# Optimization experiments

Measured on AMD Instinct MI355X. Metric: run time of the kernel, lower is better.

## Reference

```python
import jax, jax.numpy as jnp
import numpy as np
from jax import lax

SCALE = 1.0 / np.sqrt(1500.0)  # self.dim = sqrt(1500)


def conv1d(x, w, b, stride, padding):
    # x: [B, Cin, L], w: [Cout, Cin, K] (torch layout)
    y = lax.conv_general_dilated(x, w, (stride,), padding,
                                 dimension_numbers=('NCH', 'OIH', 'NCH'))
    return y + b[None, :, None]


def setup_inputs() -> dict:
    key = jax.random.key(0)
    ks = jax.random.split(key, 16)
    B, L, F = 32, 1500, 8  # feature_len = 8, seq len pinned by sqrt(1500) and logit=Linear(176,3)

    def n(k, shape, s=0.1):
        return jax.random.normal(k, shape, jnp.float32) * s

    return {
        'signal': jax.random.normal(ks[0], (B, 1, L), jnp.float32),
        # first (and only executed) head: kernel_size = 3, padding 'same'
        'wq': n(ks[1], (F, 1, 3)), 'bq': n(ks[2], (F,)),
        'wk': n(ks[3], (F, 1, 3)), 'bk': n(ks[4], (F,)),
        'wv': n(ks[5], (F, 1, 3)), 'bv': n(ks[6], (F,)),
        # final conv stack (finetune path): 1500 -> 374 -> 92 -> 22
        'w1': n(ks[7], (32, F, 8)),  'b1': n(ks[8], (32,)),
        'w2': n(ks[9], (64, 32, 8)), 'b2': n(ks[10], (64,)),
        'w3': n(ks[11], (F, 64, 8)), 'b3': n(ks[12], (F,)),
        # logit: Linear(176, 3); 176 = 8 * 22
        'wl': n(ks[13], (3, 176)), 'bl': n(ks[14], (3,)),
    }


def reference(signal, wq, bq, wk, bk, wv, bv, w1, b1, w2, b2, w3, b3, wl, bl):
    # conv QKV projections (kernel 3, 'same' padding), each [B, 8, L]
    Q = conv1d(signal, wq, bq, 1, 'SAME')
    K = conv1d(signal, wk, bk, 1, 'SAME')
    V = conv1d(signal, wv, bv, 1, 'SAME')
    # score = bmm(Q^T, K) / sqrt(1500)  -> [B, L, L]
    score = jnp.einsum('bcl,bcm->blm', Q, K) * SCALE
    attn = jax.nn.softmax(score, axis=-1)
    # context = bmm(attn, V^T)^T -> [B, 8, L]
    context = jnp.einsum('blm,bcm->bcl', attn, V)
    # finetune head: three strided convs (no activations in the original)
    h = conv1d(context, w1, b1, 4, 'VALID')  # [B, 32, 374]
    h = conv1d(h, w2, b2, 4, 'VALID')        # [B, 64, 92]
    h = conv1d(h, w3, b3, 4, 'VALID')        # [B, 8, 22]
    flat = h.reshape(h.shape[0], -1)          # [B, 176]
    return flat @ wl.T + bl                   # [B, 3]
```

## Files before the change

### kernel.cpp

```cpp
#include <hip/hip_runtime.h>

#define F_SCALE 0.02581988897471611f
#define F_LOG2E 1.4426950408889634f

constexpr int B_ = 32;
constexpr int L_ = 1500;
constexpr int LP_ = 1504;
constexpr int MSPLIT = 16;
constexpr int MCHUNK = 94;

constexpr size_t OFF_PS   = 0;
constexpr size_t SZ_PS    = (size_t)B_ * MSPLIT * 4 * LP_;
constexpr size_t OFF_CTX  = OFF_PS + SZ_PS;
constexpr size_t SZ_CTX   = (size_t)B_ * 8 * LP_;
constexpr size_t OFF_H1   = OFF_CTX + SZ_CTX;
constexpr size_t SZ_H1    = (size_t)B_ * 32 * 376;
constexpr size_t OFF_H2   = OFF_H1 + SZ_H1;
constexpr size_t SZ_H2    = (size_t)B_ * 64 * 96;

__global__ __launch_bounds__(256, 6) void attn_partial(
    const float* __restrict__ signal,
    const float* __restrict__ wq, const float* __restrict__ bq,
    const float* __restrict__ wk,
    float* __restrict__ ps)
{
    __shared__ float  sigp[LP_];
    __shared__ float4 gArr[MCHUNK];

    const int tid = threadIdx.x;
    const int lt  = blockIdx.x;
    const int ms  = blockIdx.y;
    const int b   = blockIdx.z;
    const int m0  = ms * MCHUNK;
    const int mcount = min(MCHUNK, L_ - m0);

    const float* sgb = signal + (size_t)b * L_;
    for (int i = tid; i < LP_; i += 256)
        sigp[i] = (i >= 1 && i <= L_) ? sgb[i - 1] : 0.0f;

    float Mm[9], uu[3];
    #pragma unroll
    for (int a = 0; a < 3; a++) {
        #pragma unroll
        for (int d = 0; d < 3; d++) {
            float acc = 0.0f;
            #pragma unroll
            for (int c = 0; c < 8; c++) acc += wq[c*3+a] * wk[c*3+d];
            Mm[a*3+d] = acc * (F_SCALE * F_LOG2E);
        }
    }
    #pragma unroll
    for (int d = 0; d < 3; d++) {
        float acc = 0.0f;
        #pragma unroll
        for (int c = 0; c < 8; c++) acc += bq[c] * wk[c*3+d];
        uu[d] = acc * (F_SCALE * F_LOG2E);
    }
    __syncthreads();

    for (int j = tid; j < mcount; j += 256) {
        const int m = m0 + j;
        const float x0 = sigp[m], x1 = sigp[m+1], x2 = sigp[m+2];
        float4 g;
        g.x = Mm[0]*x0 + Mm[1]*x1 + Mm[2]*x2;
        g.y = Mm[3]*x0 + Mm[4]*x1 + Mm[5]*x2;
        g.z = Mm[6]*x0 + Mm[7]*x1 + Mm[8]*x2;
        g.w = uu[0]*x0 + uu[1]*x1 + uu[2]*x2;
        gArr[j] = g;
    }
    __syncthreads();

    const int l0 = lt * 512 + tid;
    const int l1 = l0 + 256;
    const bool has1 = (l1 < L_);
    const int l1c = has1 ? l1 : (L_ - 1);

    const float xa0 = sigp[l0],  xa1 = sigp[l0+1],  xa2 = sigp[l0+2];
    const float xb0 = sigp[l1c], xb1 = sigp[l1c+1], xb2 = sigp[l1c+2];

    float S0a=0,S1a=0,S2a=0,Da=0, S0b=0,S1b=0,S2b=0,Db=0;
    float sa = sigp[m0], sb = sigp[m0+1];

    #pragma unroll 4
    for (int j = 0; j < mcount; j++) {
        const float4 g = gArr[j];
        const float sc = sigp[m0 + j + 2];
        const float s_a = fmaf(xa0, g.x, fmaf(xa1, g.y, fmaf(xa2, g.z, g.w)));
        const float s_b = fmaf(xb0, g.x, fmaf(xb1, g.y, fmaf(xb2, g.z, g.w)));
        const float pa = __builtin_amdgcn_exp2f(s_a);
        const float pb = __builtin_amdgcn_exp2f(s_b);
        Da += pa; Db += pb;
        S0a = fmaf(pa, sa, S0a); S1a = fmaf(pa, sb, S1a); S2a = fmaf(pa, sc, S2a);
        S0b = fmaf(pb, sa, S0b); S1b = fmaf(pb, sb, S1b); S2b = fmaf(pb, sc, S2b);
        sa = sb; sb = sc;
    }

    float* pc = ps + ((size_t)(b * MSPLIT + ms) * 4) * LP_;
    pc[0*LP_+l0]=S0a; pc[1*LP_+l0]=S1a; pc[2*LP_+l0]=S2a; pc[3*LP_+l0]=Da;
    if (has1) {
        pc[0*LP_+l1]=S0b; pc[1*LP_+l1]=S1b; pc[2*LP_+l1]=S2b; pc[3*LP_+l1]=Db;
    }
}

__global__ __launch_bounds__(256) void attn_combine(
    const float* __restrict__ ps,
    const float* __restrict__ wv, const float* __restrict__ bv,
    float* __restrict__ ctx)
{
    const int l = blockIdx.x * 256 + threadIdx.x;
    const int b = blockIdx.y;
    if (l >= L_) return;
    float S0=0, S1=0, S2=0, D=0;
    #pragma unroll
    for (int s = 0; s < MSPLIT; s++) {
        const float* base = ps + ((size_t)(b*MSPLIT + s) * 4) * LP_ + l;
        S0 += base[0*LP_]; S1 += base[1*LP_]; S2 += base[2*LP_]; D += base[3*LP_];
    }
    const float rd = 1.0f / D;
    #pragma unroll
    for (int c = 0; c < 8; c++) {
        ctx[((size_t)b * 8 + c) * LP_ + l] =
            (wv[c*3+0]*S0 + wv[c*3+1]*S1 + wv[c*3+2]*S2) * rd + bv[c];
    }
}

__global__ __launch_bounds__(192) void conv1k(
    const float* __restrict__ ctx, const float* __restrict__ w1,
    const float* __restrict__ b1, float* __restrict__ h1)
{
    const int t = blockIdx.x * 192 + threadIdx.x;
    const int o = blockIdx.y, b = blockIdx.z;
    if (t >= 374) return;
    float acc = b1[o];
    const float4* cb = reinterpret_cast<const float4*>(ctx + (size_t)b * 8 * LP_);
    const float* w = w1 + o * 64;
    #pragma unroll
    for (int i = 0; i < 8; i++) {
        const float4 a0 = cb[i * 376 + t];
        const float4 a1 = cb[i * 376 + t + 1];
        acc += a0.x*w[i*8+0] + a0.y*w[i*8+1] + a0.z*w[i*8+2] + a0.w*w[i*8+3]
             + a1.x*w[i*8+4] + a1.y*w[i*8+5] + a1.z*w[i*8+6] + a1.w*w[i*8+7];
    }
    h1[((size_t)b * 32 + o) * 376 + t] = acc;
}

__global__ __launch_bounds__(128) void conv2k(
    const float* __restrict__ h1, const float* __restrict__ w2,
    const float* __restrict__ b2, float* __restrict__ h2)
{
    const int t = threadIdx.x;
    const int o = blockIdx.x, b = blockIdx.y;
    if (t >= 92) return;
    float acc = b2[o];
    const float4* hb = reinterpret_cast<const float4*>(h1 + (size_t)b * 32 * 376);
    const float* w = w2 + o * 256;
    #pragma unroll 8
    for (int i = 0; i < 32; i++) {
        const float4 a0 = hb[i * 94 + t];
        const float4 a1 = hb[i * 94 + t + 1];
        acc += a0.x*w[i*8+0] + a0.y*w[i*8+1] + a0.z*w[i*8+2] + a0.w*w[i*8+3]
             + a1.x*w[i*8+4] + a1.y*w[i*8+5] + a1.z*w[i*8+6] + a1.w*w[i*8+7];
    }
    h2[((size_t)b * 64 + o) * 96 + t] = acc;
}

__global__ __launch_bounds__(192) void conv3_logit(
    const float* __restrict__ h2, const float* __restrict__ w3,
    const float* __restrict__ b3, const float* __restrict__ wl,
    const float* __restrict__ bl, float* __restrict__ out)
{
    __shared__ float flat[176];
    const int tid = threadIdx.x, b = blockIdx.x;
    if (tid < 176) {
        const int c = tid / 22, t = tid % 22;
        float acc = b3[c];
        const float4* hb = reinterpret_cast<const float4*>(h2 + (size_t)b * 64 * 96);
        #pragma unroll 8
        for (int i = 0; i < 64; i++) {
            const float4 a0 = hb[i * 24 + t];
            const float4 a1 = hb[i * 24 + t + 1];
            const float* w = w3 + (c * 64 + i) * 8;
            acc += a0.x*w[0] + a0.y*w[1] + a0.z*w[2] + a0.w*w[3]
                 + a1.x*w[4] + a1.y*w[5] + a1.z*w[6] + a1.w*w[7];
        }
        flat[tid] = acc;
    }
    __syncthreads();
    if (tid < 3) {
        float acc = bl[tid];
        for (int n = 0; n < 176; n++) acc += flat[n] * wl[tid * 176 + n];
        out[b * 3 + tid] = acc;
    }
}

extern "C" void kernel_launch(void* const* d_in, const int* in_sizes, int n_in,
                              void* d_out, int out_size, void* d_ws, size_t ws_size,
                              hipStream_t stream) {
    const float* signal = (const float*)d_in[0];
    const float* wq = (const float*)d_in[1];  const float* bq = (const float*)d_in[2];
    const float* wk = (const float*)d_in[3];
    const float* wv = (const float*)d_in[5];  const float* bv = (const float*)d_in[6];
    const float* w1 = (const float*)d_in[7];  const float* b1 = (const float*)d_in[8];
    const float* w2 = (const float*)d_in[9];  const float* b2 = (const float*)d_in[10];
    const float* w3 = (const float*)d_in[11]; const float* b3 = (const float*)d_in[12];
    const float* wl = (const float*)d_in[13]; const float* bl = (const float*)d_in[14];
    float* out = (float*)d_out;

    float* ws  = (float*)d_ws;
    float* ps  = ws + OFF_PS;
    float* ctx = ws + OFF_CTX;
    float* h1  = ws + OFF_H1;
    float* h2  = ws + OFF_H2;

    hipLaunchKernelGGL(attn_partial, dim3(3, MSPLIT, 32), dim3(256), 0, stream,
                       signal, wq, bq, wk, ps);
    hipLaunchKernelGGL(attn_combine, dim3(6, 32), dim3(256), 0, stream, ps, wv, bv, ctx);
    hipLaunchKernelGGL(conv1k, dim3(2, 32, 32), dim3(192), 0, stream, ctx, w1, b1, h1);
    hipLaunchKernelGGL(conv2k, dim3(64, 32), dim3(128), 0, stream, h1, w2, b2, h2);
    hipLaunchKernelGGL(conv3_logit, dim3(32), dim3(192), 0, stream, h2, w3, b3, wl, bl, out);
}
```

Baseline: 145.2 us.

## Fuse attention combine with first conv and fold V projection into conv weights

```diff
diff --git a/kernel.cpp b/kernel.cpp
--- a/kernel.cpp
+++ b/kernel.cpp
@@ -11,9 +11,7 @@
 
 constexpr size_t OFF_PS   = 0;
 constexpr size_t SZ_PS    = (size_t)B_ * MSPLIT * 4 * LP_;
-constexpr size_t OFF_CTX  = OFF_PS + SZ_PS;
-constexpr size_t SZ_CTX   = (size_t)B_ * 8 * LP_;
-constexpr size_t OFF_H1   = OFF_CTX + SZ_CTX;
+constexpr size_t OFF_H1   = OFF_PS + SZ_PS;
 constexpr size_t SZ_H1    = (size_t)B_ * 32 * 376;
 constexpr size_t OFF_H2   = OFF_H1 + SZ_H1;
 constexpr size_t SZ_H2    = (size_t)B_ * 64 * 96;
@@ -102,46 +100,68 @@
     }
 }
 
-__global__ __launch_bounds__(256) void attn_combine(
+__global__ __launch_bounds__(256) void fused_ctx_conv1(
     const float* __restrict__ ps,
     const float* __restrict__ wv, const float* __restrict__ bv,
-    float* __restrict__ ctx)
-{
-    const int l = blockIdx.x * 256 + threadIdx.x;
-    const int b = blockIdx.y;
-    if (l >= L_) return;
-    float S0=0, S1=0, S2=0, D=0;
-    #pragma unroll
-    for (int s = 0; s < MSPLIT; s++) {
-        const float* base = ps + ((size_t)(b*MSPLIT + s) * 4) * LP_ + l;
-        S0 += base[0*LP_]; S1 += base[1*LP_]; S2 += base[2*LP_]; D += base[3*LP_];
-    }
-    const float rd = 1.0f / D;
-    #pragma unroll
-    for (int c = 0; c < 8; c++) {
-        ctx[((size_t)b * 8 + c) * LP_ + l] =
-            (wv[c*3+0]*S0 + wv[c*3+1]*S1 + wv[c*3+2]*S2) * rd + bv[c];
-    }
-}
-
-__global__ __launch_bounds__(192) void conv1k(
-    const float* __restrict__ ctx, const float* __restrict__ w1,
-    const float* __restrict__ b1, float* __restrict__ h1)
-{
-    const int t = blockIdx.x * 192 + threadIdx.x;
-    const int o = blockIdx.y, b = blockIdx.z;
-    if (t >= 374) return;
-    float acc = b1[o];
-    const float4* cb = reinterpret_cast<const float4*>(ctx + (size_t)b * 8 * LP_);
-    const float* w = w1 + o * 64;
+    const float* __restrict__ w1, const float* __restrict__ b1,
+    float* __restrict__ h1)
+{
+    __shared__ float4 TD[192];
+    const int tid = threadIdx.x;
+    const int xb  = blockIdx.x;
+    const int b   = blockIdx.y;
+    const int t0  = xb * 47;
+    const int ncols = min(47, 374 - t0);
+    const int lbase = 4 * t0;
+
+    if (tid < 192) {
+        const int l = lbase + tid;
+        float S0=0, S1=0, S2=0, D=1.0f;
+        if (l < L_) {
+            const float* base = ps + ((size_t)b * MSPLIT * 4) * LP_ + l;
+            D = 0.0f;
+            #pragma unroll
+            for (int s = 0; s < MSPLIT; s++) {
+                const float* p = base + (size_t)s * 4 * LP_;
+                S0 += p[0*LP_]; S1 += p[1*LP_]; S2 += p[2*LP_]; D += p[3*LP_];
+            }
+        }
+        const float rd = 1.0f / D;
+        TD[tid] = make_float4(S0*rd, S1*rd, S2*rd, 0.0f);
+    }
+
+    const int o = tid & 31;
+    float A[8][3];
+    float b1p = b1[o];
+    #pragma unroll
+    for (int k = 0; k < 8; k++) { A[k][0]=0.f; A[k][1]=0.f; A[k][2]=0.f; }
     #pragma unroll
     for (int i = 0; i < 8; i++) {
-        const float4 a0 = cb[i * 376 + t];
-        const float4 a1 = cb[i * 376 + t + 1];
-        acc += a0.x*w[i*8+0] + a0.y*w[i*8+1] + a0.z*w[i*8+2] + a0.w*w[i*8+3]
-             + a1.x*w[i*8+4] + a1.y*w[i*8+5] + a1.z*w[i*8+6] + a1.w*w[i*8+7];
-    }
-    h1[((size_t)b * 32 + o) * 376 + t] = acc;
+        const float v0 = wv[i*3+0], v1 = wv[i*3+1], v2 = wv[i*3+2];
+        const float bvi = bv[i];
+        #pragma unroll
+        for (int k = 0; k < 8; k++) {
+            const float w = w1[o*64 + i*8 + k];
+            A[k][0] = fmaf(w, v0, A[k][0]);
+            A[k][1] = fmaf(w, v1, A[k][1]);
+            A[k][2] = fmaf(w, v2, A[k][2]);
+            b1p     = fmaf(w, bvi, b1p);
+        }
+    }
+    __syncthreads();
+
+    const int g = tid >> 5;
+    float* hb = h1 + ((size_t)b * 32 + o) * 376;
+    for (int t = g; t < ncols; t += 8) {
+        float acc = b1p;
+        const int li = 4 * t;
+        #pragma unroll
+        for (int k = 0; k < 8; k++) {
+            const float4 T = TD[li + k];
+            acc += A[k][0]*T.x + A[k][1]*T.y + A[k][2]*T.z;
+        }
+        hb[t0 + t] = acc;
+    }
 }
 
 __global__ __launch_bounds__(128) void conv2k(
@@ -206,16 +226,15 @@
     const float* wl = (const float*)d_in[13]; const float* bl = (const float*)d_in[14];
     float* out = (float*)d_out;
 
-    float* ws  = (float*)d_ws;
-    float* ps  = ws + OFF_PS;
-    float* ctx = ws + OFF_CTX;
-    float* h1  = ws + OFF_H1;
-    float* h2  = ws + OFF_H2;
+    float* ws = (float*)d_ws;
+    float* ps = ws + OFF_PS;
+    float* h1 = ws + OFF_H1;
+    float* h2 = ws + OFF_H2;
 
     hipLaunchKernelGGL(attn_partial, dim3(3, MSPLIT, 32), dim3(256), 0, stream,
                        signal, wq, bq, wk, ps);
-    hipLaunchKernelGGL(attn_combine, dim3(6, 32), dim3(256), 0, stream, ps, wv, bv, ctx);
-    hipLaunchKernelGGL(conv1k, dim3(2, 32, 32), dim3(192), 0, stream, ctx, w1, b1, h1);
+    hipLaunchKernelGGL(fused_ctx_conv1, dim3(8, 32), dim3(256), 0, stream,
+                       ps, wv, bv, w1, b1, h1);
     hipLaunchKernelGGL(conv2k, dim3(64, 32), dim3(128), 0, stream, h1, w2, b2, h2);
     hipLaunchKernelGGL(conv3_logit, dim3(32), dim3(192), 0, stream, h2, w3, b3, wl, bl, out);
 }
```

New measurement: 142.8 us. Within noise of the previous version (-1.6%).
